# Performance work log

Hardware: AMD Instinct MI355X
Metric: run time of the kernel (lower is better)

The kernel has to match this reference:

```python
import jax, jax.numpy as jnp
import numpy as np

B, N, D, L, T = 64, 64, 6, 32, 2048
RHO = 0.7
W = np.float32(RHO ** (1.0 / L))  # per-step decay, rho ** (1/l_patts)


def setup_inputs() -> dict:
    key = jax.random.key(0)
    k1, k2 = jax.random.split(key)
    x = jax.random.normal(k1, (B, D, T), dtype=jnp.float32)
    patts = jax.random.normal(k2, (N, L), dtype=jnp.float32)  # torch.randn(n_patts, l_patts)
    w = jnp.float32(W)
    return {"x": x, "patts": patts, "w": w}


def _dtw_sq(x, patts, w):
    """Open-end (subsequence) weighted DTW of each pattern against each channel.

    DP recurrence (squared-distance cost, decay w on accumulated path):
      D[0, j] = c[0, j]                                    (free start in time)
      D[i, j] = c[i, j] + w * min(D[i-1, j], D[i, j-1], D[i-1, j-1])
    Output O[b, n, d, j] = D[L-1, j]  (distance of full pattern ending at time j).
    """
    b, d, t = x.shape
    n, l = patts.shape
    is_first = jnp.arange(l) == 0  # (L,)

    def col_step(Dprev_t, xt):
        # Dprev_t: (L, B, N, D) previous time column; xt: (B, D)
        # cost c[i] = (patts[n, i] - x[b, d, j])^2 -> (L, B, N, D)
        c_t = (patts.T[:, None, :, None] - xt[None, :, None, :]) ** 2
        Dprev_im1 = jnp.concatenate(
            [jnp.full_like(Dprev_t[:1], jnp.inf), Dprev_t[:-1]], axis=0)

        def cell(d_im1, inputs):
            ci, dp_i, dp_im1, first = inputs
            m = jnp.minimum(jnp.minimum(dp_i, dp_im1), d_im1)
            di = jnp.where(first, ci, ci + w * m)
            return di, di

        init = jnp.full(Dprev_t.shape[1:], jnp.inf, x.dtype)
        _, Dcol_t = jax.lax.scan(cell, init, (c_t, Dprev_t, Dprev_im1, is_first))
        return Dcol_t, Dcol_t[-1]  # carry full column, emit last row D[L-1, j]

    Dinit = jnp.full((l, b, n, d), jnp.inf, x.dtype)
    xs = jnp.moveaxis(x, -1, 0)  # (T, B, D)
    _, last = jax.lax.scan(col_step, Dinit, xs)  # (T, B, N, D)
    return jnp.moveaxis(last, 0, -1)  # (B, N, D, T)


def reference(x, patts, w):
    return jnp.sqrt(_dtw_sq(x, patts, w))
```

## Files before the change

### kernel.cpp

```cpp
#include <hip/hip_runtime.h>
#include <math.h>

#define TB 2048
#define LL 32
#define NP 64
#define DD 6
#define BB 64
#define CW 16
#define MSTEPS (TB/CW)
#define XSTRIDE 20


__device__ __forceinline__ float dpp_shr1(float v) {
    const int i = __float_as_int(v);
    const int r = __builtin_amdgcn_update_dpp(i, i, 0x111, 0xF, 0xF, false);
    return __int_as_float(r);
}

#define STEP(XV, Y) {                                        \
    const float up = dpp_shr1(Y);                            \
    const float t0 = p0 - (XV);                              \
    const float t1 = p1 - (XV);                              \
    const float t2 = p2 - (XV);                              \
    const float t3 = p3 - (XV);                              \
    const float c0 = t0 * t0;                                \
    const float m0 = fminf(fminf(a0, up), diag);             \
    const float v0 = k0 ? c0 : fmaf(w, m0, c0);              \
    const float m1 = fminf(fminf(a1, v0), a0);               \
    const float v1 = fmaf(w, m1, t1 * t1);                   \
    const float m2 = fminf(fminf(a2, v1), a1);               \
    const float v2 = fmaf(w, m2, t2 * t2);                   \
    const float m3 = fminf(fminf(a3, v2), a2);               \
    const float v3 = fmaf(w, m3, t3 * t3);                   \
    a0 = v0; a1 = v1; a2 = v2; a3 = v3;                      \
    diag = up;                                               \
    Y = v3;                                                  \
}

__global__ __launch_bounds__(64, 3) void dtw_kernel(
    const float* __restrict__ x,
    const float* __restrict__ patts,
    const float* __restrict__ wptr,
    float* __restrict__ out)
{
    __shared__ float xs[MSTEPS * XSTRIDE];

    const int bid = blockIdx.x;
    const int oct = bid & 7;
    const int bd  = bid >> 3;
    const int tid = threadIdx.x;

    const float INF = __builtin_inff();

    const float4* xrow = (const float4*)(x + (size_t)bd * TB);
    #pragma unroll
    for (int i = 0; i < 8; ++i) {
        const int idx = tid + i * 64;
        *(float4*)(xs + (idx >> 2) * XSTRIDE + (idx & 3) * 4) = xrow[idx];
    }
    __syncthreads();

    const int g = tid >> 3;
    const int k = tid & 7;
    const int n = oct * 8 + g;

    const float w = wptr[0];
    const float4 pv = *(const float4*)(patts + n * LL + k * 4);
    const float p0 = pv.x, p1 = pv.y, p2 = pv.z, p3 = pv.w;

    const int b = bd / DD, d = bd - (bd / DD) * DD;
    float* __restrict__ orow = out + (((size_t)b * NP + n) * DD + d) * TB;

    const bool k0 = (k == 0), k7 = (k == 7);

    float a0 = INF, a1 = INF, a2 = INF, a3 = INF;
    float diag = INF;
    float y0 = INF, y1 = INF, y2 = INF, y3 = INF,
          y4 = INF, y5 = INF, y6 = INF, y7 = INF,
          y8 = INF, y9 = INF, y10 = INF, y11 = INF,
          y12 = INF, y13 = INF, y14 = INF, y15 = INF;

    for (int m = 0; m < MSTEPS + 7; ++m) {
        const int q = m - k;
        const bool valid = ((unsigned)q < (unsigned)MSTEPS);
        const int qq = valid ? q : 0;
        const float* xb = xs + qq * XSTRIDE;

        const float4 xA = *(const float4*)(xb + 0);
        const float4 xB = *(const float4*)(xb + 4);
        const float4 xC = *(const float4*)(xb + 8);
        const float4 xD = *(const float4*)(xb + 12);

        STEP(xA.x, y0)  STEP(xA.y, y1)  STEP(xA.z, y2)  STEP(xA.w, y3)
        STEP(xB.x, y4)  STEP(xB.y, y5)  STEP(xB.z, y6)  STEP(xB.w, y7)
        STEP(xC.x, y8)  STEP(xC.y, y9)  STEP(xC.z, y10) STEP(xC.w, y11)
        STEP(xD.x, y12) STEP(xD.y, y13) STEP(xD.z, y14) STEP(xD.w, y15)

        if (k7 && valid) {
            float4* op = (float4*)(orow + q * CW);
            op[0] = make_float4(sqrtf(y0),  sqrtf(y1),  sqrtf(y2),  sqrtf(y3));
            op[1] = make_float4(sqrtf(y4),  sqrtf(y5),  sqrtf(y6),  sqrtf(y7));
            op[2] = make_float4(sqrtf(y8),  sqrtf(y9),  sqrtf(y10), sqrtf(y11));
            op[3] = make_float4(sqrtf(y12), sqrtf(y13), sqrtf(y14), sqrtf(y15));
        }
    }
}

extern "C" void kernel_launch(void* const* d_in, const int* in_sizes, int n_in,
                              void* d_out, int out_size, void* d_ws, size_t ws_size,
                              hipStream_t stream) {
    const float* x     = (const float*)d_in[0];
    const float* patts = (const float*)d_in[1];
    const float* wptr  = (const float*)d_in[2];
    float* out = (float*)d_out;

    dim3 grid(BB * DD * 8);
    dim3 block(64);
    dtw_kernel<<<grid, block, 0, stream>>>(x, patts, wptr, out);
}
```

Measured before the change: 364.8 us.

## Split each pattern across 16 lanes with 2 rows each, 256-thread blocks

Each pattern's 32 DP rows are now split over 16 lanes of 2 rows each instead of 8 lanes of 4 rows. Each block has 256 threads covering 16 patterns, and the grid is 4 blocks per (b,d) row. This shortens the serial per-lane dependency chain per time step, but lengthens the wavefront skew to 15 steps and doubles the number of DPP shifts per useful cell. The sqrt calls are also replaced with the raw hardware sqrt builtin, which is cheaper but less precise.

```diff
diff --git a/kernel.cpp b/kernel.cpp
--- a/kernel.cpp
+++ b/kernel.cpp
@@ -8,6 +8,8 @@
 #define BB 64
 #define CW 16
 #define MSTEPS (TB/CW)
+#define NL 16
+#define RW 2
 #define XSTRIDE 20
 
 
@@ -17,27 +19,21 @@
     return __int_as_float(r);
 }
 
-#define STEP(XV, Y) {                                        \
+#define STEP2(XV, Y) {                                       \
     const float up = dpp_shr1(Y);                            \
     const float t0 = p0 - (XV);                              \
     const float t1 = p1 - (XV);                              \
-    const float t2 = p2 - (XV);                              \
-    const float t3 = p3 - (XV);                              \
     const float c0 = t0 * t0;                                \
     const float m0 = fminf(fminf(a0, up), diag);             \
-    const float v0 = k0 ? c0 : fmaf(w, m0, c0);              \
+    const float f0 = fmaf(w, m0, c0);                        \
+    const float v0 = k0 ? c0 : f0;                           \
     const float m1 = fminf(fminf(a1, v0), a0);               \
     const float v1 = fmaf(w, m1, t1 * t1);                   \
-    const float m2 = fminf(fminf(a2, v1), a1);               \
-    const float v2 = fmaf(w, m2, t2 * t2);                   \
-    const float m3 = fminf(fminf(a3, v2), a2);               \
-    const float v3 = fmaf(w, m3, t3 * t3);                   \
-    a0 = v0; a1 = v1; a2 = v2; a3 = v3;                      \
-    diag = up;                                               \
-    Y = v3;                                                  \
+    a0 = v0; a1 = v1; diag = up;                             \
+    Y = v1;                                                  \
 }
 
-__global__ __launch_bounds__(64, 3) void dtw_kernel(
+__global__ __launch_bounds__(256) void dtw_kernel(
     const float* __restrict__ x,
     const float* __restrict__ patts,
     const float* __restrict__ wptr,
@@ -45,42 +41,42 @@
 {
     __shared__ float xs[MSTEPS * XSTRIDE];
 
-    const int bid = blockIdx.x;
-    const int oct = bid & 7;
-    const int bd  = bid >> 3;
-    const int tid = threadIdx.x;
+    const int bid  = blockIdx.x;
+    const int quad = bid & 3;
+    const int bd   = bid >> 2;
+    const int tid  = threadIdx.x;
 
     const float INF = __builtin_inff();
 
     const float4* xrow = (const float4*)(x + (size_t)bd * TB);
     #pragma unroll
-    for (int i = 0; i < 8; ++i) {
-        const int idx = tid + i * 64;
+    for (int i = 0; i < 2; ++i) {
+        const int idx = tid + i * 256;
         *(float4*)(xs + (idx >> 2) * XSTRIDE + (idx & 3) * 4) = xrow[idx];
     }
     __syncthreads();
 
-    const int g = tid >> 3;
-    const int k = tid & 7;
-    const int n = oct * 8 + g;
+    const int g = tid >> 4;
+    const int k = tid & 15;
+    const int n = quad * 16 + g;
 
     const float w = wptr[0];
-    const float4 pv = *(const float4*)(patts + n * LL + k * 4);
-    const float p0 = pv.x, p1 = pv.y, p2 = pv.z, p3 = pv.w;
+    const float2 pv = *(const float2*)(patts + n * LL + k * RW);
+    const float p0 = pv.x, p1 = pv.y;
 
     const int b = bd / DD, d = bd - (bd / DD) * DD;
     float* __restrict__ orow = out + (((size_t)b * NP + n) * DD + d) * TB;
 
-    const bool k0 = (k == 0), k7 = (k == 7);
+    const bool k0 = (k == 0), kl = (k == NL - 1);
 
-    float a0 = INF, a1 = INF, a2 = INF, a3 = INF;
+    float a0 = INF, a1 = INF;
     float diag = INF;
     float y0 = INF, y1 = INF, y2 = INF, y3 = INF,
           y4 = INF, y5 = INF, y6 = INF, y7 = INF,
           y8 = INF, y9 = INF, y10 = INF, y11 = INF,
           y12 = INF, y13 = INF, y14 = INF, y15 = INF;
 
-    for (int m = 0; m < MSTEPS + 7; ++m) {
+    for (int m = 0; m < MSTEPS + NL - 1; ++m) {
         const int q = m - k;
         const bool valid = ((unsigned)q < (unsigned)MSTEPS);
         const int qq = valid ? q : 0;
@@ -91,17 +87,29 @@
         const float4 xC = *(const float4*)(xb + 8);
         const float4 xD = *(const float4*)(xb + 12);
 
-        STEP(xA.x, y0)  STEP(xA.y, y1)  STEP(xA.z, y2)  STEP(xA.w, y3)
-        STEP(xB.x, y4)  STEP(xB.y, y5)  STEP(xB.z, y6)  STEP(xB.w, y7)
-        STEP(xC.x, y8)  STEP(xC.y, y9)  STEP(xC.z, y10) STEP(xC.w, y11)
-        STEP(xD.x, y12) STEP(xD.y, y13) STEP(xD.z, y14) STEP(xD.w, y15)
+        STEP2(xA.x, y0)  STEP2(xA.y, y1)  STEP2(xA.z, y2)  STEP2(xA.w, y3)
+        STEP2(xB.x, y4)  STEP2(xB.y, y5)  STEP2(xB.z, y6)  STEP2(xB.w, y7)
+        STEP2(xC.x, y8)  STEP2(xC.y, y9)  STEP2(xC.z, y10) STEP2(xC.w, y11)
+        STEP2(xD.x, y12) STEP2(xD.y, y13) STEP2(xD.z, y14) STEP2(xD.w, y15)
 
-        if (k7 && valid) {
+        if (kl && valid) {
             float4* op = (float4*)(orow + q * CW);
-            op[0] = make_float4(sqrtf(y0),  sqrtf(y1),  sqrtf(y2),  sqrtf(y3));
-            op[1] = make_float4(sqrtf(y4),  sqrtf(y5),  sqrtf(y6),  sqrtf(y7));
-            op[2] = make_float4(sqrtf(y8),  sqrtf(y9),  sqrtf(y10), sqrtf(y11));
-            op[3] = make_float4(sqrtf(y12), sqrtf(y13), sqrtf(y14), sqrtf(y15));
+            op[0] = make_float4(__builtin_amdgcn_sqrtf(y0),
+                                __builtin_amdgcn_sqrtf(y1),
+                                __builtin_amdgcn_sqrtf(y2),
+                                __builtin_amdgcn_sqrtf(y3));
+            op[1] = make_float4(__builtin_amdgcn_sqrtf(y4),
+                                __builtin_amdgcn_sqrtf(y5),
+                                __builtin_amdgcn_sqrtf(y6),
+                                __builtin_amdgcn_sqrtf(y7));
+            op[2] = make_float4(__builtin_amdgcn_sqrtf(y8),
+                                __builtin_amdgcn_sqrtf(y9),
+                                __builtin_amdgcn_sqrtf(y10),
+                                __builtin_amdgcn_sqrtf(y11));
+            op[3] = make_float4(__builtin_amdgcn_sqrtf(y12),
+                                __builtin_amdgcn_sqrtf(y13),
+                                __builtin_amdgcn_sqrtf(y14),
+                                __builtin_amdgcn_sqrtf(y15));
         }
     }
 }
@@ -114,7 +122,7 @@
     const float* wptr  = (const float*)d_in[2];
     float* out = (float*)d_out;
 
-    dim3 grid(BB * DD * 8);
-    dim3 block(64);
+    dim3 grid(BB * DD * 4);
+    dim3 block(256);
     dtw_kernel<<<grid, block, 0, stream>>>(x, patts, wptr, out);
 }
```

Measured after the change: 322.5 us. -11.6%, faster.
